# Optimization experiments

Hardware: AMD Instinct MI355X
Metric: run time of the kernel (lower is better)

Reference implementation:

```python
import jax, jax.numpy as jnp
import numpy as np

EPS = 1e-12


def agnn_layer(x, row, col, num_nodes):
    """AGNN propagation with beta frozen at 1.0 (requires_grad=False in source).
    alpha_ij = softmax_{j in N(i)} ( beta * cos(x_i, x_j) ); out_i = sum_j alpha_ij * x_j.
    row = destination node of each edge (segment id), col = source node.
    """
    xn = x / (jnp.linalg.norm(x, axis=-1, keepdims=True) + EPS)  # unit-norm features
    score = jnp.sum(xn[row] * xn[col], axis=-1)                   # [E] beta=1 * cos sim
    smax = jax.ops.segment_max(score, row, num_segments=num_nodes)
    e = jnp.exp(score - smax[row])                                # stable softmax numerator
    denom = jax.ops.segment_sum(e, row, num_segments=num_nodes)
    alpha = e / jnp.maximum(denom[row], EPS)                      # [E]
    out = jax.ops.segment_sum(alpha[:, None] * x[col], row, num_segments=num_nodes)
    return out


def setup_inputs() -> dict:
    key = jax.random.key(0)
    ks = jax.random.split(key, 8)
    N, E = 100000, 1600000
    IN_DIM, HID, OUT_DIM = 128, 64, 64
    x = jax.random.normal(ks[0], (N, IN_DIM), dtype=jnp.float32)
    edge_row = jnp.sort(jax.random.randint(ks[1], (E,), 0, N))
    edge_col = jax.random.randint(ks[2], (E,), 0, N)
    # Linear params (PyTorch nn.Linear style: y = x @ W.T + b)
    s1 = 1.0 / np.sqrt(IN_DIM)
    W1 = jax.random.uniform(ks[3], (HID, IN_DIM), jnp.float32, -s1, s1)
    b1 = jax.random.uniform(ks[4], (HID,), jnp.float32, -s1, s1)
    s2 = 1.0 / np.sqrt(HID)
    W2 = jax.random.uniform(ks[5], (OUT_DIM, HID), jnp.float32, -s2, s2)
    b2 = jax.random.uniform(ks[6], (OUT_DIM,), jnp.float32, -s2, s2)
    return {"x": x, "edge_row": edge_row, "edge_col": edge_col,
            "W1": W1, "b1": b1, "W2": W2, "b2": b2}


def reference(x, edge_row, edge_col, W1, b1, W2, b2):
    N = x.shape[0]
    h = jax.nn.relu(x @ W1.T + b1)
    for _ in range(4):  # 4 frozen-beta AGNN layers
        h = jax.nn.relu(agnn_layer(h, edge_row, edge_col, N))
    return h @ W2.T + b2
```

## Files before the change

kernel.cpp:

```cpp
#include <hip/hip_runtime.h>


typedef _Float16 h2 __attribute__((ext_vector_type(2)));

union U4H { uint4 u; h2 h[4]; };
union U2H { uint2 u; h2 h[2]; };
union UHI { unsigned u; h2 h; };
union UF  { unsigned u; float f; int i; };

#define DEV_INLINE __device__ __forceinline__

DEV_INLINE h2 mkh2(float a, float b) {
    h2 r; r.x = (_Float16)a; r.y = (_Float16)b; return r;
}

template <int CTRL>
DEV_INLINE float dpp_addf(float x) {
    UF a, b;
    a.f = x;
    b.i = __builtin_amdgcn_update_dpp(0, a.i, CTRL, 0xF, 0xF, true);
    return x + b.f;
}

__global__ __launch_bounds__(256) void build_rowptr_scan(const int* __restrict__ row,
                                                         int* __restrict__ ptr,
                                                         int N, int E) {
    int e = blockIdx.x * blockDim.x + threadIdx.x;
    if (e >= E) return;
    const int r1 = row[e];
    const int r0 = (e == 0) ? -1 : row[e - 1];
    for (int i = r0 + 1; i <= r1; ++i) ptr[i] = e;
    if (e == E - 1) {
        for (int i = r1 + 1; i <= N; ++i) ptr[i] = E;
    }
}

#define PSEG 1024
__global__ __launch_bounds__(1024) void build_perm_seg(const int* __restrict__ ptr,
                                                       int4* __restrict__ meta,
                                                       int N) {
    __shared__ int hist[256];
    __shared__ int tmp[256];
    const int t    = threadIdx.x;
    const int base = blockIdx.x * PSEG;
    const int end  = (base + PSEG < N) ? base + PSEG : N;
    const int cnt  = end - base;

    if (t < 256) hist[t] = 0;
    __syncthreads();

    int d = -1, p0v = 0, p1v = 0;
    if (t < cnt) {
        p0v = ptr[base + t];
        p1v = ptr[base + t + 1];
        d = p1v - p0v;
        if (d > 255) d = 255;
        atomicAdd(&hist[d], 1);
    }
    __syncthreads();

    int h0 = (t < 256) ? hist[t] : 0;
    int* src = hist; int* dst = tmp;
    for (int off = 1; off < 256; off <<= 1) {
        if (t < 256) dst[t] = src[t] + (t >= off ? src[t - off] : 0);
        __syncthreads();
        int* tt = src; src = dst; dst = tt;
    }
    if (t < 256) src[t] -= h0;
    __syncthreads();

    if (t < cnt) {
        int pos = base + atomicAdd(&src[d], 1);
        meta[pos] = make_int4(base + t, p0v, p1v, 0);
    }
}

#define GEMM_BODY4(w4, xv)                                      \
    acc[0].x = fmaf(xv.x, w4.x, acc[0].x);                      \
    acc[0].y = fmaf(xv.x, w4.y, acc[0].y);                      \
    acc[0].z = fmaf(xv.x, w4.z, acc[0].z);                      \
    acc[0].w = fmaf(xv.x, w4.w, acc[0].w);                      \
    acc[1].x = fmaf(xv.y, w4.x, acc[1].x);                      \
    acc[1].y = fmaf(xv.y, w4.y, acc[1].y);                      \
    acc[1].z = fmaf(xv.y, w4.z, acc[1].z);                      \
    acc[1].w = fmaf(xv.y, w4.w, acc[1].w);                      \
    acc[2].x = fmaf(xv.z, w4.x, acc[2].x);                      \
    acc[2].y = fmaf(xv.z, w4.y, acc[2].y);                      \
    acc[2].z = fmaf(xv.z, w4.z, acc[2].z);                      \
    acc[2].w = fmaf(xv.z, w4.w, acc[2].w);                      \
    acc[3].x = fmaf(xv.w, w4.x, acc[3].x);                      \
    acc[3].y = fmaf(xv.w, w4.y, acc[3].y);                      \
    acc[3].z = fmaf(xv.w, w4.z, acc[3].z);                      \
    acc[3].w = fmaf(xv.w, w4.w, acc[3].w);

__global__ __launch_bounds__(256) void gemm1_relu(const float* __restrict__ x,
                                                  const float* __restrict__ W1,
                                                  const float* __restrict__ b1,
                                                  unsigned short* __restrict__ xn,
                                                  float* __restrict__ nrm,
                                                  int N) {
    __shared__ __align__(16) float Wt[32 * 64];
    __shared__ __align__(16) float xT[32 * 64];
    const int tid  = threadIdx.x;
    const int tx   = tid & 15;
    const int ty   = tid >> 4;
    const int base = blockIdx.x * 64;

    const float4* W4  = (const float4*)W1;
    const float4* x4p = (const float4*)x;

    const int wO  = tid & 63;
    const int wK4 = tid >> 6;
    const int nodeA = base + wO;
    const bool okA  = nodeA < N;

    float4 wv0, wv1, xv0, xv1;
    wv0 = W4[wO * 32 + wK4];
    wv1 = W4[wO * 32 + 4 + wK4];
    xv0 = make_float4(0.f, 0.f, 0.f, 0.f);
    xv1 = xv0;
    if (okA) {
        xv0 = x4p[(size_t)nodeA * 32 + wK4];
        xv1 = x4p[(size_t)nodeA * 32 + 4 + wK4];
    }

    float4 b4 = ((const float4*)b1)[tx];
    float4 acc[4];
    acc[0] = b4; acc[1] = b4; acc[2] = b4; acc[3] = b4;

    for (int c = 0; c < 4; ++c) {
        Wt[(4 * wK4 + 0) * 64 + wO] = wv0.x;
        Wt[(4 * wK4 + 1) * 64 + wO] = wv0.y;
        Wt[(4 * wK4 + 2) * 64 + wO] = wv0.z;
        Wt[(4 * wK4 + 3) * 64 + wO] = wv0.w;
        Wt[(4 * (wK4 + 4) + 0) * 64 + wO] = wv1.x;
        Wt[(4 * (wK4 + 4) + 1) * 64 + wO] = wv1.y;
        Wt[(4 * (wK4 + 4) + 2) * 64 + wO] = wv1.z;
        Wt[(4 * (wK4 + 4) + 3) * 64 + wO] = wv1.w;
        xT[(4 * wK4 + 0) * 64 + wO] = xv0.x;
        xT[(4 * wK4 + 1) * 64 + wO] = xv0.y;
        xT[(4 * wK4 + 2) * 64 + wO] = xv0.z;
        xT[(4 * wK4 + 3) * 64 + wO] = xv0.w;
        xT[(4 * (wK4 + 4) + 0) * 64 + wO] = xv1.x;
        xT[(4 * (wK4 + 4) + 1) * 64 + wO] = xv1.y;
        xT[(4 * (wK4 + 4) + 2) * 64 + wO] = xv1.z;
        xT[(4 * (wK4 + 4) + 3) * 64 + wO] = xv1.w;
        __syncthreads();

        if (c < 3) {
            const int ko = (c + 1) * 8;
            wv0 = W4[wO * 32 + ko + wK4];
            wv1 = W4[wO * 32 + ko + 4 + wK4];
            if (okA) {
                xv0 = x4p[(size_t)nodeA * 32 + ko + wK4];
                xv1 = x4p[(size_t)nodeA * 32 + ko + 4 + wK4];
            }
        }

#pragma unroll 4
        for (int k = 0; k < 32; ++k) {
            const float4 w4 = *(const float4*)&Wt[k * 64 + 4 * tx];
            const float4 xv = *(const float4*)&xT[k * 64 + 4 * ty];
            GEMM_BODY4(w4, xv)
        }
        if (c < 3) __syncthreads();
    }

#pragma unroll
    for (int mm = 0; mm < 4; ++mm) {
        float4 r = acc[mm];
        r.x = fmaxf(r.x, 0.f); r.y = fmaxf(r.y, 0.f);
        r.z = fmaxf(r.z, 0.f); r.w = fmaxf(r.w, 0.f);
        float s = fmaf(r.x, r.x, fmaf(r.y, r.y, fmaf(r.z, r.z, r.w * r.w)));
        s = dpp_addf<0xB1>(s);
        s = dpp_addf<0x4E>(s);
        s = dpp_addf<0x141>(s);
        s = dpp_addf<0x140>(s);
        const float nn  = sqrtf(s) + 1e-12f;
        const float inv = 1.f / nn;
        int node = base + 4 * ty + mm;
        if (node < N) {
            U2H pk;
            pk.h[0] = mkh2(r.x * inv, r.y * inv);
            pk.h[1] = mkh2(r.z * inv, r.w * inv);
            *(uint2*)&xn[(size_t)node * 64 + 4 * tx] = pk.u;
            if (tx == mm) nrm[node] = nn;
        }
    }
}

__global__ __launch_bounds__(256, 6) void agnn_layer(const uint4* __restrict__ xn4,
                                                     const float* __restrict__ nrm,
                                                     const int4* __restrict__ meta,
                                                     const int* __restrict__ col,
                                                     uint4* __restrict__ xo4,
                                                     float* __restrict__ nrmo,
                                                     int N) {
    const int tid  = threadIdx.x;
    const int lane = tid & 63;
    const int g    = (lane >> 3) & 1;
    const int sub  = lane & 7;
    const int slot = blockIdx.x * 16 + (tid >> 4);
    if (slot >= N) return;

    const int4 m0 = meta[slot];
    const int i  = m0.x;
    const int p0 = m0.y, p1 = m0.z;

    U4H hi_;
    hi_.u = xn4[(unsigned)i * 8u + sub];
    {
        const _Float16 L2E = (_Float16)1.4426950408889634f;
        h2 l2 = {L2E, L2E};
#pragma unroll
        for (int c = 0; c < 4; ++c) hi_.h[c] *= l2;
    }

    const int mid = p0 + ((p1 - p0 + 1) >> 1);
    int       t   = g ? mid : p0;
    const int e_  = g ? p1  : mid;

    float den = 0.f;
    U4H acc;
    acc.h[0] = mkh2(0.f, 0.f); acc.h[1] = mkh2(0.f, 0.f);
    acc.h[2] = mkh2(0.f, 0.f); acc.h[3] = mkh2(0.f, 0.f);

    for (; t < e_; t += 8) {
        const int nb = e_ - t;
        int   jj[8];
        uint4 v[8];
        float nm[8];

#pragma unroll
        for (int k = 0; k < 8; ++k) {
            int e = t + k;
            e = (e < e_) ? e : (e_ - 1);
            jj[k] = col[e];
        }
#pragma unroll
        for (int k = 0; k < 8; ++k) v[k] = xn4[(unsigned)jj[k] * 8u + sub];
#pragma unroll
        for (int k = 0; k < 8; ++k) nm[k] = nrm[jj[k]];

#pragma unroll
        for (int k = 0; k < 8; ++k) {
            U4H xa; xa.u = v[k];
            float sa = __builtin_amdgcn_fdot2(hi_.h[0], xa.h[0], 0.f, false);
            sa = __builtin_amdgcn_fdot2(hi_.h[1], xa.h[1], sa, false);
            float sb = __builtin_amdgcn_fdot2(hi_.h[2], xa.h[2], 0.f, false);
            sb = __builtin_amdgcn_fdot2(hi_.h[3], xa.h[3], sb, false);
            float s = sa + sb;
            s = dpp_addf<0xB1>(s);
            s = dpp_addf<0x4E>(s);
            s = dpp_addf<0x141>(s);
            const float p = (k < nb) ? exp2f(s) : 0.f;
            den += p;
            const _Float16 wh = (_Float16)(p * nm[k]);
            h2 w2 = {wh, wh};
            acc.h[0] += w2 * xa.h[0];
            acc.h[1] += w2 * xa.h[1];
            acc.h[2] += w2 * xa.h[2];
            acc.h[3] += w2 * xa.h[3];
        }
    }

    den = dpp_addf<0x140>(den);
#pragma unroll
    for (int c = 0; c < 4; ++c) {
        UHI a; a.h = acc.h[c];
        UHI b; b.u = (unsigned)__shfl_xor((int)a.u, 8, 64);
        acc.h[c] = a.h + b.h;
    }

    const float id = 1.f / fmaxf(den, 1e-12f);
    float o[8];
#pragma unroll
    for (int c = 0; c < 4; ++c) {
        o[2 * c]     = fmaxf((float)acc.h[c].x * id, 0.f);
        o[2 * c + 1] = fmaxf((float)acc.h[c].y * id, 0.f);
    }

    float s2 = 0.f;
#pragma unroll
    for (int c = 0; c < 8; ++c) s2 = fmaf(o[c], o[c], s2);
    s2 = dpp_addf<0xB1>(s2);
    s2 = dpp_addf<0x4E>(s2);
    s2 = dpp_addf<0x141>(s2);
    const float nn  = sqrtf(s2) + 1e-12f;
    const float inv = 1.f / nn;

    if (g == 0) {
        U4H ov;
        ov.h[0] = mkh2(o[0] * inv, o[1] * inv);
        ov.h[1] = mkh2(o[2] * inv, o[3] * inv);
        ov.h[2] = mkh2(o[4] * inv, o[5] * inv);
        ov.h[3] = mkh2(o[6] * inv, o[7] * inv);
        xo4[(unsigned)i * 8u + sub] = ov.u;
        if (sub == 0) nrmo[i] = nn;
    }
}

__global__ __launch_bounds__(256) void gemm2(const unsigned short* __restrict__ xn,
                                             const float* __restrict__ nrm,
                                             const float* __restrict__ W2,
                                             const float* __restrict__ b2,
                                             float* __restrict__ out,
                                             int N) {
    __shared__ __align__(16) float Wt[64 * 64];
    __shared__ __align__(16) float xT[64 * 64];
    const int tid  = threadIdx.x;
    const int tx   = tid & 15;
    const int ty   = tid >> 4;
    const int base = blockIdx.x * 64;

    {
        const float4* W4 = (const float4*)W2;
#pragma unroll
        for (int it = 0; it < 4; ++it) {
            int idx = tid + it * 256;
            int o = idx & 63, k4 = idx >> 6;
            float4 v = W4[o * 16 + k4];
            Wt[(4 * k4 + 0) * 64 + o] = v.x;
            Wt[(4 * k4 + 1) * 64 + o] = v.y;
            Wt[(4 * k4 + 2) * 64 + o] = v.z;
            Wt[(4 * k4 + 3) * 64 + o] = v.w;
        }
        const uint2* x2 = (const uint2*)xn;
#pragma unroll
        for (int it = 0; it < 4; ++it) {
            int idx = tid + it * 256;
            int mm = idx & 63, k4 = idx >> 6;
            int node = base + mm;
            U2H v; v.u = make_uint2(0u, 0u);
            float nn = 0.f;
            if (node < N) { v.u = x2[(size_t)node * 16 + k4]; nn = nrm[node]; }
            xT[(4 * k4 + 0) * 64 + mm] = (float)v.h[0].x * nn;
            xT[(4 * k4 + 1) * 64 + mm] = (float)v.h[0].y * nn;
            xT[(4 * k4 + 2) * 64 + mm] = (float)v.h[1].x * nn;
            xT[(4 * k4 + 3) * 64 + mm] = (float)v.h[1].y * nn;
        }
    }
    __syncthreads();

    float4 b4 = ((const float4*)b2)[tx];
    float4 acc[4];
    acc[0] = b4; acc[1] = b4; acc[2] = b4; acc[3] = b4;

#pragma unroll 4
    for (int k = 0; k < 64; ++k) {
        const float4 w4 = *(const float4*)&Wt[k * 64 + 4 * tx];
        const float4 xv = *(const float4*)&xT[k * 64 + 4 * ty];
        GEMM_BODY4(w4, xv)
    }

#pragma unroll
    for (int mm = 0; mm < 4; ++mm) {
        int node = base + 4 * ty + mm;
        if (node < N) *(float4*)&out[(size_t)node * 64 + 4 * tx] = acc[mm];
    }
}

extern "C" void kernel_launch(void* const* d_in, const int* in_sizes, int n_in,
                              void* d_out, int out_size, void* d_ws, size_t ws_size,
                              hipStream_t stream) {
    const float* x   = (const float*)d_in[0];
    const int*   row = (const int*)d_in[1];
    const int*   col = (const int*)d_in[2];
    const float* W1  = (const float*)d_in[3];
    const float* b1  = (const float*)d_in[4];
    const float* W2  = (const float*)d_in[5];
    const float* b2  = (const float*)d_in[6];
    float* out = (float*)d_out;

    const int N = in_sizes[0] / 128;
    const int E = in_sizes[1];

    char* ws = (char*)d_ws;
    size_t off = 0;
    unsigned short* ha = (unsigned short*)(ws + off); off += (size_t)N * 64 * 2;
    unsigned short* hb = (unsigned short*)(ws + off); off += (size_t)N * 64 * 2;
    float* na_  = (float*)(ws + off); off += (size_t)N * sizeof(float);
    float* nb_  = (float*)(ws + off); off += (size_t)N * sizeof(float);
    int*   ptr  = (int*)  (ws + off); off += (size_t)(N + 1) * sizeof(int);
    off = (off + 15) & ~(size_t)15;
    int4*  meta = (int4*) (ws + off); off += (size_t)N * sizeof(int4);
    (void)ws_size; (void)n_in; (void)out_size;

    build_rowptr_scan<<<(E + 255) / 256, 256, 0, stream>>>(row, ptr, N, E);

    build_perm_seg<<<(N + PSEG - 1) / PSEG, 1024, 0, stream>>>(ptr, meta, N);

    const int nbG = (N + 63) / 64;
    gemm1_relu<<<nbG, 256, 0, stream>>>(x, W1, b1, ha, na_, N);

    const int nb16 = (N + 15) / 16;
    unsigned short* hc = ha; unsigned short* hn = hb;
    float* nc = na_; float* nn = nb_;
    for (int l = 0; l < 4; ++l) {
        agnn_layer<<<nb16, 256, 0, stream>>>((const uint4*)hc, nc, meta, col,
                                             (uint4*)hn, nn, N);
        unsigned short* t = hc; hc = hn; hn = t;
        float* tf = nc; nc = nn; nn = tf;
    }

    gemm2<<<nbG, 256, 0, stream>>>(hc, nc, W2, b2, out, N);
}
```

Baseline: 296.8 us.

## Fuse last AGNN layer with output GEMM and build row pointers via binary search

Replaces the row-pointer scan kernel with per-node binary searches over the sorted row array inside the meta-building kernel, removing one launch and the ptr buffer. Fuses the fourth AGNN layer with the final linear layer: each block keeps its 16 node outputs in shared memory and multiplies them by a transposed W2 staged in LDS. This skips writing and re-reading the fp16 hidden state and its norms. The trade-off is that every block of the fused kernel reloads W2 into LDS and uses more shared memory, which may reduce occupancy.

```diff
diff --git a/kernel.cpp b/kernel.cpp
--- a/kernel.cpp
+++ b/kernel.cpp
@@ -22,23 +22,11 @@
     return x + b.f;
 }
 
-__global__ __launch_bounds__(256) void build_rowptr_scan(const int* __restrict__ row,
-                                                         int* __restrict__ ptr,
-                                                         int N, int E) {
-    int e = blockIdx.x * blockDim.x + threadIdx.x;
-    if (e >= E) return;
-    const int r1 = row[e];
-    const int r0 = (e == 0) ? -1 : row[e - 1];
-    for (int i = r0 + 1; i <= r1; ++i) ptr[i] = e;
-    if (e == E - 1) {
-        for (int i = r1 + 1; i <= N; ++i) ptr[i] = E;
-    }
-}
-
 #define PSEG 1024
-__global__ __launch_bounds__(1024) void build_perm_seg(const int* __restrict__ ptr,
-                                                       int4* __restrict__ meta,
-                                                       int N) {
+__global__ __launch_bounds__(1024) void build_meta_sort(const int* __restrict__ row,
+                                                        int4* __restrict__ meta,
+                                                        int N, int E) {
+    __shared__ int ptr_s[PSEG + 1];
     __shared__ int hist[256];
     __shared__ int tmp[256];
     const int t    = threadIdx.x;
@@ -46,13 +34,31 @@
     const int end  = (base + PSEG < N) ? base + PSEG : N;
     const int cnt  = end - base;
 
+    if (t < cnt) {
+        const int target = base + t;
+        int lo = 0, hi = E;
+        while (lo < hi) {
+            int mid = (lo + hi) >> 1;
+            if (row[mid] < target) lo = mid + 1; else hi = mid;
+        }
+        ptr_s[t] = lo;
+    }
+    if (t == 0) {
+        const int target = end;
+        int lo = 0, hi = E;
+        while (lo < hi) {
+            int mid = (lo + hi) >> 1;
+            if (row[mid] < target) lo = mid + 1; else hi = mid;
+        }
+        ptr_s[cnt] = lo;
+    }
     if (t < 256) hist[t] = 0;
     __syncthreads();
 
     int d = -1, p0v = 0, p1v = 0;
     if (t < cnt) {
-        p0v = ptr[base + t];
-        p1v = ptr[base + t + 1];
+        p0v = ptr_s[t];
+        p1v = ptr_s[t + 1];
         d = p1v - p0v;
         if (d > 255) d = 255;
         atomicAdd(&hist[d], 1);
@@ -189,6 +195,44 @@
     }
 }
 
+#define AGNN_EDGE_LOOP()                                                     \
+    for (; t < e_; t += 8) {                                                 \
+        const int nb = e_ - t;                                               \
+        int   jj[8];                                                         \
+        uint4 v[8];                                                          \
+        float nm[8];                                                         \
+        _Pragma("unroll")                                                    \
+        for (int k = 0; k < 8; ++k) {                                        \
+            int e = t + k;                                                   \
+            e = (e < e_) ? e : (e_ - 1);                                     \
+            jj[k] = col[e];                                                  \
+        }                                                                    \
+        _Pragma("unroll")                                                    \
+        for (int k = 0; k < 8; ++k) v[k] = xn4[(unsigned)jj[k] * 8u + sub];  \
+        _Pragma("unroll")                                                    \
+        for (int k = 0; k < 8; ++k) nm[k] = nrm[jj[k]];                      \
+        _Pragma("unroll")                                                    \
+        for (int k = 0; k < 8; ++k) {                                        \
+            U4H xa; xa.u = v[k];                                             \
+            float sa = __builtin_amdgcn_fdot2(hi_.h[0], xa.h[0], 0.f, false);\
+            sa = __builtin_amdgcn_fdot2(hi_.h[1], xa.h[1], sa, false);       \
+            float sb = __builtin_amdgcn_fdot2(hi_.h[2], xa.h[2], 0.f, false);\
+            sb = __builtin_amdgcn_fdot2(hi_.h[3], xa.h[3], sb, false);       \
+            float s = sa + sb;                                               \
+            s = dpp_addf<0xB1>(s);                                           \
+            s = dpp_addf<0x4E>(s);                                           \
+            s = dpp_addf<0x141>(s);                                          \
+            const float p = (k < nb) ? exp2f(s) : 0.f;                       \
+            den += p;                                                        \
+            const _Float16 wh = (_Float16)(p * nm[k]);                       \
+            h2 w2 = {wh, wh};                                                \
+            acc.h[0] += w2 * xa.h[0];                                        \
+            acc.h[1] += w2 * xa.h[1];                                        \
+            acc.h[2] += w2 * xa.h[2];                                        \
+            acc.h[3] += w2 * xa.h[3];                                        \
+        }                                                                    \
+    }
+
 __global__ __launch_bounds__(256, 6) void agnn_layer(const uint4* __restrict__ xn4,
                                                      const float* __restrict__ nrm,
                                                      const int4* __restrict__ meta,
@@ -225,44 +269,7 @@
     acc.h[0] = mkh2(0.f, 0.f); acc.h[1] = mkh2(0.f, 0.f);
     acc.h[2] = mkh2(0.f, 0.f); acc.h[3] = mkh2(0.f, 0.f);
 
-    for (; t < e_; t += 8) {
-        const int nb = e_ - t;
-        int   jj[8];
-        uint4 v[8];
-        float nm[8];
-
-#pragma unroll
-        for (int k = 0; k < 8; ++k) {
-            int e = t + k;
-            e = (e < e_) ? e : (e_ - 1);
-            jj[k] = col[e];
-        }
-#pragma unroll
-        for (int k = 0; k < 8; ++k) v[k] = xn4[(unsigned)jj[k] * 8u + sub];
-#pragma unroll
-        for (int k = 0; k < 8; ++k) nm[k] = nrm[jj[k]];
-
-#pragma unroll
-        for (int k = 0; k < 8; ++k) {
-            U4H xa; xa.u = v[k];
-            float sa = __builtin_amdgcn_fdot2(hi_.h[0], xa.h[0], 0.f, false);
-            sa = __builtin_amdgcn_fdot2(hi_.h[1], xa.h[1], sa, false);
-            float sb = __builtin_amdgcn_fdot2(hi_.h[2], xa.h[2], 0.f, false);
-            sb = __builtin_amdgcn_fdot2(hi_.h[3], xa.h[3], sb, false);
-            float s = sa + sb;
-            s = dpp_addf<0xB1>(s);
-            s = dpp_addf<0x4E>(s);
-            s = dpp_addf<0x141>(s);
-            const float p = (k < nb) ? exp2f(s) : 0.f;
-            den += p;
-            const _Float16 wh = (_Float16)(p * nm[k]);
-            h2 w2 = {wh, wh};
-            acc.h[0] += w2 * xa.h[0];
-            acc.h[1] += w2 * xa.h[1];
-            acc.h[2] += w2 * xa.h[2];
-            acc.h[3] += w2 * xa.h[3];
-        }
-    }
+    AGNN_EDGE_LOOP()
 
     den = dpp_addf<0x140>(den);
 #pragma unroll
@@ -300,63 +307,114 @@
     }
 }
 
-__global__ __launch_bounds__(256) void gemm2(const unsigned short* __restrict__ xn,
-                                             const float* __restrict__ nrm,
-                                             const float* __restrict__ W2,
-                                             const float* __restrict__ b2,
-                                             float* __restrict__ out,
-                                             int N) {
-    __shared__ __align__(16) float Wt[64 * 64];
-    __shared__ __align__(16) float xT[64 * 64];
+__global__ __launch_bounds__(256, 6) void agnn_gemm2(const uint4* __restrict__ xn4,
+                                                     const float* __restrict__ nrm,
+                                                     const int4* __restrict__ meta,
+                                                     const int* __restrict__ col,
+                                                     const float* __restrict__ W2,
+                                                     const float* __restrict__ b2,
+                                                     float* __restrict__ out,
+                                                     int N) {
+    __shared__ __align__(16) float W2T[64 * 68];
+    __shared__ __align__(16) float oL[16][68];
     const int tid  = threadIdx.x;
-    const int tx   = tid & 15;
-    const int ty   = tid >> 4;
-    const int base = blockIdx.x * 64;
+    const int lane = tid & 63;
+    const int g    = (lane >> 3) & 1;
+    const int sub  = lane & 7;
+    const int q    = tid >> 4;
+    const int il   = tid & 15;
+    const int slot = blockIdx.x * 16 + q;
+    const bool slotOK = slot < N;
 
     {
-        const float4* W4 = (const float4*)W2;
-#pragma unroll
-        for (int it = 0; it < 4; ++it) {
-            int idx = tid + it * 256;
-            int o = idx & 63, k4 = idx >> 6;
-            float4 v = W4[o * 16 + k4];
-            Wt[(4 * k4 + 0) * 64 + o] = v.x;
-            Wt[(4 * k4 + 1) * 64 + o] = v.y;
-            Wt[(4 * k4 + 2) * 64 + o] = v.z;
-            Wt[(4 * k4 + 3) * 64 + o] = v.w;
-        }
-        const uint2* x2 = (const uint2*)xn;
-#pragma unroll
-        for (int it = 0; it < 4; ++it) {
-            int idx = tid + it * 256;
-            int mm = idx & 63, k4 = idx >> 6;
-            int node = base + mm;
-            U2H v; v.u = make_uint2(0u, 0u);
-            float nn = 0.f;
-            if (node < N) { v.u = x2[(size_t)node * 16 + k4]; nn = nrm[node]; }
-            xT[(4 * k4 + 0) * 64 + mm] = (float)v.h[0].x * nn;
-            xT[(4 * k4 + 1) * 64 + mm] = (float)v.h[0].y * nn;
-            xT[(4 * k4 + 2) * 64 + mm] = (float)v.h[1].x * nn;
-            xT[(4 * k4 + 3) * 64 + mm] = (float)v.h[1].y * nn;
-        }
-    }
+        const float4* src = (const float4*)W2;
+#pragma unroll
+        for (int i2 = 0; i2 < 4; ++i2) {
+            int idx = tid + i2 * 256;
+            int j = idx >> 4, k4 = idx & 15;
+            float4 v = src[idx];
+            W2T[(4 * k4 + 0) * 68 + j] = v.x;
+            W2T[(4 * k4 + 1) * 68 + j] = v.y;
+            W2T[(4 * k4 + 2) * 68 + j] = v.z;
+            W2T[(4 * k4 + 3) * 68 + j] = v.w;
+        }
+    }
+
+    int nid = 0;
+    if (slotOK) {
+        const int4 m0 = meta[slot];
+        nid = m0.x;
+        const int p0 = m0.y, p1 = m0.z;
+        const int i = nid;
+
+        U4H hi_;
+        hi_.u = xn4[(unsigned)i * 8u + sub];
+        {
+            const _Float16 L2E = (_Float16)1.4426950408889634f;
+            h2 l2 = {L2E, L2E};
+#pragma unroll
+            for (int c = 0; c < 4; ++c) hi_.h[c] *= l2;
+        }
+
+        const int mid = p0 + ((p1 - p0 + 1) >> 1);
+        int       t   = g ? mid : p0;
+        const int e_  = g ? p1  : mid;
+
+        float den = 0.f;
+        U4H acc;
+        acc.h[0] = mkh2(0.f, 0.f); acc.h[1] = mkh2(0.f, 0.f);
+        acc.h[2] = mkh2(0.f, 0.f); acc.h[3] = mkh2(0.f, 0.f);
+
+        AGNN_EDGE_LOOP()
+
+        den = dpp_addf<0x140>(den);
+#pragma unroll
+        for (int c = 0; c < 4; ++c) {
+            UHI a; a.h = acc.h[c];
+            UHI b; b.u = (unsigned)__shfl_xor((int)a.u, 8, 64);
+            acc.h[c] = a.h + b.h;
+        }
+
+        const float id = 1.f / fmaxf(den, 1e-12f);
+        float o[8];
+#pragma unroll
+        for (int c = 0; c < 4; ++c) {
+            o[2 * c]     = fmaxf((float)acc.h[c].x * id, 0.f);
+            o[2 * c + 1] = fmaxf((float)acc.h[c].y * id, 0.f);
+        }
+
+        if (g == 0) {
+            oL[q][8 * sub + 0] = o[0];
+            oL[q][8 * sub + 1] = o[1];
+            oL[q][8 * sub + 2] = o[2];
+            oL[q][8 * sub + 3] = o[3];
+            oL[q][8 * sub + 4] = o[4];
+            oL[q][8 * sub + 5] = o[5];
+            oL[q][8 * sub + 6] = o[6];
+            oL[q][8 * sub + 7] = o[7];
+        }
+    }
+
     __syncthreads();
 
-    float4 b4 = ((const float4*)b2)[tx];
-    float4 acc[4];
-    acc[0] = b4; acc[1] = b4; acc[2] = b4; acc[3] = b4;
-
+    if (slotOK) {
+        float4 res = ((const float4*)b2)[il];
 #pragma unroll 4
-    for (int k = 0; k < 64; ++k) {
-        const float4 w4 = *(const float4*)&Wt[k * 64 + 4 * tx];
-        const float4 xv = *(const float4*)&xT[k * 64 + 4 * ty];
-        GEMM_BODY4(w4, xv)
-    }
-
-#pragma unroll
-    for (int mm = 0; mm < 4; ++mm) {
-        int node = base + 4 * ty + mm;
-        if (node < N) *(float4*)&out[(size_t)node * 64 + 4 * tx] = acc[mm];
+        for (int kk = 0; kk < 16; ++kk) {
+            const float4 o4 = *(const float4*)&oL[q][4 * kk];
+#pragma unroll
+            for (int c = 0; c < 4; ++c) {
+                const int k = 4 * kk + c;
+                const float4 w4 = *(const float4*)&W2T[k * 68 + 4 * il];
+                const float ok = (c == 0) ? o4.x : (c == 1) ? o4.y
+                               : (c == 2) ? o4.z : o4.w;
+                res.x = fmaf(ok, w4.x, res.x);
+                res.y = fmaf(ok, w4.y, res.y);
+                res.z = fmaf(ok, w4.z, res.z);
+                res.w = fmaf(ok, w4.w, res.w);
+            }
+        }
+        *(float4*)&out[(size_t)nid * 64 + 4 * il] = res;
     }
 }
 
@@ -381,14 +439,11 @@
     unsigned short* hb = (unsigned short*)(ws + off); off += (size_t)N * 64 * 2;
     float* na_  = (float*)(ws + off); off += (size_t)N * sizeof(float);
     float* nb_  = (float*)(ws + off); off += (size_t)N * sizeof(float);
-    int*   ptr  = (int*)  (ws + off); off += (size_t)(N + 1) * sizeof(int);
     off = (off + 15) & ~(size_t)15;
     int4*  meta = (int4*) (ws + off); off += (size_t)N * sizeof(int4);
     (void)ws_size; (void)n_in; (void)out_size;
 
-    build_rowptr_scan<<<(E + 255) / 256, 256, 0, stream>>>(row, ptr, N, E);
-
-    build_perm_seg<<<(N + PSEG - 1) / PSEG, 1024, 0, stream>>>(ptr, meta, N);
+    build_meta_sort<<<(N + PSEG - 1) / PSEG, 1024, 0, stream>>>(row, meta, N, E);
 
     const int nbG = (N + 63) / 64;
     gemm1_relu<<<nbG, 256, 0, stream>>>(x, W1, b1, ha, na_, N);
@@ -396,12 +451,13 @@
     const int nb16 = (N + 15) / 16;
     unsigned short* hc = ha; unsigned short* hn = hb;
     float* nc = na_; float* nn = nb_;
-    for (int l = 0; l < 4; ++l) {
+    for (int l = 0; l < 3; ++l) {
         agnn_layer<<<nb16, 256, 0, stream>>>((const uint4*)hc, nc, meta, col,
                                              (uint4*)hn, nn, N);
         unsigned short* t = hc; hc = hn; hn = t;
         float* tf = nc; nc = nn; nn = tf;
     }
 
-    gemm2<<<nbG, 256, 0, stream>>>(hc, nc, W2, b2, out, N);
-}
+    agnn_gemm2<<<nb16, 256, 0, stream>>>((const uint4*)hc, nc, meta, col,
+                                         W2, b2, out, N);
+}
```

New measurement: 282.6 us. 4.8% less time.
